# Optimization experiments

Measured on AMD Instinct MI355X. Metric: run time of the kernel, lower is better.

The kernel has to match this reference:

```python
import jax, jax.numpy as jnp
import numpy as np

N, NA, LAYERS = 8, 4, 4
NTOT = N + NA
DIM = 2 ** NTOT
B = 1024

# Diagonal of the fixed CZ brick layer (CZ is diagonal, so one elementwise pass per layer).
# Qubit 0 is the most-significant bit of the state index (tensorcircuit convention).
def _cz_diag():
    idx = np.arange(DIM)
    bits = (idx[None, :] >> (NTOT - 1 - np.arange(NTOT)[:, None])) & 1  # [NTOT, DIM]
    par = np.zeros(DIM, dtype=np.int64)
    for i in range(NTOT // 2):
        par += bits[2 * i] * bits[2 * i + 1]
    for i in range((NTOT - 1) // 2):
        par += bits[2 * i + 1] * bits[2 * i + 2]
    return jnp.asarray(1.0 - 2.0 * (par % 2), dtype=jnp.complex64)

CZ_DIAG = _cz_diag()

def _apply_1q(state, U, q):
    # state: [B, DIM]; apply 2x2 unitary U on qubit q (batched over samples)
    l, r = 2 ** q, 2 ** (NTOT - q - 1)
    s = state.reshape(-1, l, 2, r)
    return jnp.einsum('ij,bljr->blir', U, s).reshape(-1, DIM)

def _back_circuit(state, params):
    # hardware-efficient ansatz: per layer RX,RY on every qubit, then CZ bricks
    for lay in range(LAYERS):
        off = 2 * NTOT * lay
        for q in range(NTOT):
            th = params[off + q] * 0.5
            c = jnp.cos(th).astype(jnp.complex64)
            ms = (-1j) * jnp.sin(th).astype(jnp.complex64)
            Rx = jnp.stack([jnp.stack([c, ms]), jnp.stack([ms, c])])
            state = _apply_1q(state, Rx, q)
            th = params[off + NTOT + q] * 0.5
            c, s = jnp.cos(th), jnp.sin(th)
            Ry = jnp.stack([jnp.stack([c, -s]), jnp.stack([s, c])]).astype(jnp.complex64)
            state = _apply_1q(state, Ry, q)
        state = state * CZ_DIAG
    return state

def setup_inputs() -> dict:
    key = jax.random.key(0)
    k1, k2, k3, k4 = jax.random.split(key, 4)
    return {
        'inputs_re': jax.random.normal(k1, (B, DIM), jnp.float32),
        'inputs_im': jax.random.normal(k2, (B, DIM), jnp.float32),
        'params': jax.random.normal(k3, (2 * NTOT * LAYERS,), jnp.float32),
        'u': jax.random.uniform(k4, (B,), jnp.float32),
    }

def reference(inputs_re, inputs_im, params, u):
    state = (inputs_re + 1j * inputs_im).astype(jnp.complex64)
    full = _back_circuit(state, params)                      # [B, 2^n_tot]
    s3 = full.reshape(B, 2 ** NA, 2 ** N)                    # [B, 2^na, 2^n]
    probs = jnp.sum(s3.real ** 2 + s3.imag ** 2, axis=2)     # ancilla outcome probs
    cdf = jnp.cumsum(probs, axis=1)
    thresh = u * cdf[:, -1]                                  # inverse-CDF multinomial
    m = jnp.argmax(cdf >= thresh[:, None], axis=1)           # [B] sampled outcome
    post = s3[jnp.arange(B), m]                              # [B, 2^n] collapsed state
    norm = jnp.sqrt(jnp.sum(post.real ** 2 + post.imag ** 2, axis=1, keepdims=True))
    post = post / norm
    return jnp.stack([post.real, post.imag], axis=-1)        # [B, 2^n, 2]
```

## Files before the change

kernel.cpp:

```cpp
#include <hip/hip_runtime.h>
#include <math.h>

#define NTOT   12
#define DIM    4096
#define NB     1024

typedef float v2f __attribute__((ext_vector_type(2)));

template<int G>
__device__ __forceinline__ void gate_pk(v2f (&x)[16], v2f P1, v2f P2) {
#pragma unroll
    for (int p = 0; p < 8; ++p) {
        const int j0 = ((p >> G) << (G + 1)) | (p & ((1 << G) - 1));
        const int j1 = j0 | (1 << G);
        const v2f x0 = x[j0], x1 = x[j1];
        v2f t, u;
        asm("v_pk_mul_f32 %0, %1, %2 op_sel:[1,1] op_sel_hi:[1,0] neg_hi:[1,0]"
            : "=v"(t) : "v"(P2), "v"(x1));
        asm("v_pk_fma_f32 %0, %1, %2, %0 op_sel:[1,0,0] op_sel_hi:[1,1,1] neg_lo:[1,0,0] neg_hi:[1,0,0]"
            : "+v"(t) : "v"(P1), "v"(x1));
        asm("v_pk_fma_f32 %0, %1, %2, %0 op_sel:[0,1,0] op_sel_hi:[0,0,1] neg_lo:[1,0,0]"
            : "+v"(t) : "v"(P2), "v"(x0));
        asm("v_pk_fma_f32 %0, %1, %2, %0 op_sel:[0,0,0] op_sel_hi:[0,1,1]"
            : "+v"(t) : "v"(P1), "v"(x0));
        asm("v_pk_mul_f32 %0, %1, %2 op_sel:[0,1] op_sel_hi:[0,0] neg_hi:[1,0]"
            : "=v"(u) : "v"(P2), "v"(x1));
        asm("v_pk_fma_f32 %0, %1, %2, %0 op_sel:[0,0,0] op_sel_hi:[0,1,1]"
            : "+v"(u) : "v"(P1), "v"(x1));
        asm("v_pk_fma_f32 %0, %1, %2, %0 op_sel:[1,1,0] op_sel_hi:[1,0,1] neg_hi:[1,0,0]"
            : "+v"(u) : "v"(P2), "v"(x0));
        asm("v_pk_fma_f32 %0, %1, %2, %0 op_sel:[1,0,0] op_sel_hi:[1,1,1]"
            : "+v"(u) : "v"(P1), "v"(x0));
        x[j0] = t; x[j1] = u;
    }
}

__device__ __forceinline__ float rl(float v, int l) {
    return __int_as_float(__builtin_amdgcn_readlane(__float_as_int(v), l));
}

__device__ __forceinline__ void apply4(v2f (&x)[16],
                                       float gv0, float gv1, float gv2, float gv3,
                                       int base) {
    v2f P1, P2;
#define LDCO(GL) \
    P1.x = rl(gv0, (GL)); P1.y = rl(gv1, (GL)); \
    P2.x = rl(gv2, (GL)); P2.y = rl(gv3, (GL));
    LDCO(base + 3); gate_pk<0>(x, P1, P2);
    LDCO(base + 2); gate_pk<1>(x, P1, P2);
    LDCO(base + 1); gate_pk<2>(x, P1, P2);
    LDCO(base + 0); gate_pk<3>(x, P1, P2);
#undef LDCO
}

__device__ __forceinline__ void applyCZ(v2f (&x)[16], const int (&sw)[16]) {
#pragma unroll
    for (int j = 0; j < 16; ++j) {
        x[j].x = __uint_as_float(__float_as_uint(x[j].x) ^ sw[j]);
        x[j].y = __uint_as_float(__float_as_uint(x[j].y) ^ sw[j]);
    }
}

__global__ __launch_bounds__(256, 5) void qddpm_kernel(
    const float* __restrict__ in_re,
    const float* __restrict__ in_im,
    const float* __restrict__ params,
    const float* __restrict__ uu,
    float* __restrict__ out)
{
    __shared__ v2f S[DIM];

    const int b    = blockIdx.x;
    const int t    = threadIdx.x;
    const int lane = t & 63;
    const float uval = uu[b];

    const int hsC   = (t >> 1) & 7;
    const int baseC = t * 16;
    const int tA    = t ^ ((t >> 4) & 14);
    const int baseB = (t >> 4) * 256 + (t & 15);

    v2f x[16];

    {
        const float4* re4 = (const float4*)(in_re + (size_t)b * DIM + t * 16);
        const float4* im4 = (const float4*)(in_im + (size_t)b * DIM + t * 16);
#pragma unroll
        for (int q = 0; q < 4; ++q) {
            const float4 vr = re4[q];
            const float4 vi = im4[q];
            x[4 * q + 0] = (v2f){vr.x, vi.x};
            x[4 * q + 1] = (v2f){vr.y, vi.y};
            x[4 * q + 2] = (v2f){vr.z, vi.z};
            x[4 * q + 3] = (v2f){vr.w, vi.w};
        }
    }

    float gv0 = 0.f, gv1 = 0.f, gv2 = 0.f, gv3 = 0.f;
    if (lane < 48) {
        const int lay = lane / 12, q = lane - lay * 12;
        float c1, s1, c2, s2;
        sincosf(params[lay * 24 + q] * 0.5f, &s1, &c1);
        sincosf(params[lay * 24 + 12 + q] * 0.5f, &s2, &c2);
        gv0 = c1 * c2; gv1 = c1 * s2; gv2 = s1 * s2; gv3 = s1 * c2;
    }

    int swA[16], swC[16];
#pragma unroll
    for (int j = 0; j < 16; ++j) {
        const int iC = t * 16 + j;
        swC[j] = (__popc(iC & (iC >> 1) & 0x7FF) & 1) << 31;
        const int iA = j * 256 + t;
        swA[j] = (__popc(iA & (iA >> 1) & 0x7FF) & 1) << 31;
    }

#define C_WRITE() { float4* dst = (float4*)(S + baseC); \
    _Pragma("unroll") for (int q = 0; q < 8; ++q) \
        dst[q ^ hsC] = make_float4(x[2*q].x, x[2*q].y, x[2*q+1].x, x[2*q+1].y); }
#define C_READ() { const float4* src = (const float4*)(S + baseC); \
    _Pragma("unroll") for (int q = 0; q < 8; ++q) { const float4 v = src[q ^ hsC]; \
        x[2*q] = (v2f){v.x, v.y}; x[2*q+1] = (v2f){v.z, v.w}; } }
#define B_IDX(j) (baseB + (j) * 16 + (((t & 15) ^ ((j) & 14)) - (t & 15)))
#define B_READ()  { _Pragma("unroll") for (int j = 0; j < 16; ++j) x[j] = S[B_IDX(j)]; }
#define B_WRITE() { _Pragma("unroll") for (int j = 0; j < 16; ++j) S[B_IDX(j)] = x[j]; }
#define A_READ()  { _Pragma("unroll") for (int j = 0; j < 16; ++j) x[j] = S[j * 256 + tA]; }
#define A_WRITE() { _Pragma("unroll") for (int j = 0; j < 16; ++j) S[j * 256 + tA] = x[j]; }

    apply4(x, gv0, gv1, gv2, gv3, 0 * 12 + 8);
    C_WRITE();
    __syncthreads();

    B_READ();
    apply4(x, gv0, gv1, gv2, gv3, 0 * 12 + 4);
    B_WRITE();
    __syncthreads();

    A_READ();
    apply4(x, gv0, gv1, gv2, gv3, 0 * 12 + 0);
    applyCZ(x, swA);
    apply4(x, gv0, gv1, gv2, gv3, 1 * 12 + 0);
    A_WRITE();
    __syncthreads();

    B_READ();
    apply4(x, gv0, gv1, gv2, gv3, 1 * 12 + 4);
    B_WRITE();
    __syncthreads();

    C_READ();
    apply4(x, gv0, gv1, gv2, gv3, 1 * 12 + 8);
    applyCZ(x, swC);
    apply4(x, gv0, gv1, gv2, gv3, 2 * 12 + 8);
    C_WRITE();
    __syncthreads();

    B_READ();
    apply4(x, gv0, gv1, gv2, gv3, 2 * 12 + 4);
    B_WRITE();
    __syncthreads();

    A_READ();
    apply4(x, gv0, gv1, gv2, gv3, 2 * 12 + 0);
    applyCZ(x, swA);
    apply4(x, gv0, gv1, gv2, gv3, 3 * 12 + 0);
    A_WRITE();
    __syncthreads();

    B_READ();
    apply4(x, gv0, gv1, gv2, gv3, 3 * 12 + 4);
    B_WRITE();
    __syncthreads();

    C_READ();
    apply4(x, gv0, gv1, gv2, gv3, 3 * 12 + 8);
    applyCZ(x, swC);
    C_WRITE();
    __syncthreads();

    float partial = 0.f;
#pragma unroll
    for (int q = 0; q < 32; ++q) {
        const int qq = q ^ (lane & 31);
        const int X  = (lane * 4 + (qq >> 3)) & 14;
        const float4 v = ((const float4*)S)[lane * 32 + (qq ^ (X >> 1))];
        partial = __builtin_fmaf(v.x, v.x,
                  __builtin_fmaf(v.y, v.y,
                  __builtin_fmaf(v.z, v.z,
                  __builtin_fmaf(v.w, v.w, partial))));
    }
    partial += __shfl_xor(partial, 1);
    partial += __shfl_xor(partial, 2);

    float pr[16];
#pragma unroll
    for (int g = 0; g < 16; ++g) pr[g] = __shfl(partial, g * 4);

    float cdf[16];
    float a = 0.f;
#pragma unroll
    for (int g = 0; g < 16; ++g) { a += pr[g]; cdf[g] = a; }
    const float thresh = uval * a;
    int m = 0;
#pragma unroll
    for (int g = 15; g >= 0; --g) { if (cdf[g] >= thresh) m = g; }
    float pm = pr[0];
#pragma unroll
    for (int g = 1; g < 16; ++g) { if (m == g) pm = pr[g]; }
    const float rn = 1.0f / sqrtf(pm);

    const v2f amp = S[m * 256 + tA];
    ((float2*)out)[(size_t)b * 256 + t] = make_float2(amp.x * rn, amp.y * rn);
}

extern "C" void kernel_launch(void* const* d_in, const int* in_sizes, int n_in,
                              void* d_out, int out_size, void* d_ws, size_t ws_size,
                              hipStream_t stream) {
    const float* in_re  = (const float*)d_in[0];
    const float* in_im  = (const float*)d_in[1];
    const float* params = (const float*)d_in[2];
    const float* u      = (const float*)d_in[3];
    float* out = (float*)d_out;
    qddpm_kernel<<<NB, 256, 0, stream>>>(in_re, in_im, params, u, out);
}
```

Before: 115.3 us.

## Process two batch samples per block and finish from registers

```diff
diff --git a/kernel.cpp b/kernel.cpp
--- a/kernel.cpp
+++ b/kernel.cpp
@@ -4,6 +4,7 @@
 #define NTOT   12
 #define DIM    4096
 #define NB     1024
+#define NBLK   (NB / 2)
 
 typedef float v2f __attribute__((ext_vector_type(2)));
 
@@ -61,38 +62,86 @@
     }
 }
 
-__global__ __launch_bounds__(256, 5) void qddpm_kernel(
+__device__ __forceinline__ void c_write(v2f* S, const v2f (&x)[16], int t) {
+    float4* dst = (float4*)(S + t * 16);
+    const int hsC = (t >> 1) & 7;
+#pragma unroll
+    for (int q = 0; q < 8; ++q)
+        dst[q ^ hsC] = make_float4(x[2*q].x, x[2*q].y, x[2*q+1].x, x[2*q+1].y);
+}
+__device__ __forceinline__ void c_read(const v2f* S, v2f (&x)[16], int t) {
+    const float4* src = (const float4*)(S + t * 16);
+    const int hsC = (t >> 1) & 7;
+#pragma unroll
+    for (int q = 0; q < 8; ++q) {
+        const float4 v = src[q ^ hsC];
+        x[2*q]   = (v2f){v.x, v.y};
+        x[2*q+1] = (v2f){v.z, v.w};
+    }
+}
+__device__ __forceinline__ void b_read(const v2f* S, v2f (&x)[16], int t) {
+#pragma unroll
+    for (int j = 0; j < 16; ++j)
+        x[j] = S[(t >> 4) * 256 + j * 16 + ((t & 15) ^ (j & 14))];
+}
+__device__ __forceinline__ void b_write(v2f* S, const v2f (&x)[16], int t) {
+#pragma unroll
+    for (int j = 0; j < 16; ++j)
+        S[(t >> 4) * 256 + j * 16 + ((t & 15) ^ (j & 14))] = x[j];
+}
+__device__ __forceinline__ void a_read(const v2f* S, v2f (&x)[16], int tA) {
+#pragma unroll
+    for (int j = 0; j < 16; ++j) x[j] = S[j * 256 + tA];
+}
+__device__ __forceinline__ void a_write(v2f* S, const v2f (&x)[16], int tA) {
+#pragma unroll
+    for (int j = 0; j < 16; ++j) S[j * 256 + tA] = x[j];
+}
+
+__global__ __launch_bounds__(256, 2) void qddpm_kernel(
     const float* __restrict__ in_re,
     const float* __restrict__ in_im,
     const float* __restrict__ params,
     const float* __restrict__ uu,
     float* __restrict__ out)
 {
-    __shared__ v2f S[DIM];
-
-    const int b    = blockIdx.x;
+    __shared__ v2f SA[DIM];
+    __shared__ v2f SB[DIM];
+
+    const int blk  = blockIdx.x;
     const int t    = threadIdx.x;
     const int lane = t & 63;
-    const float uval = uu[b];
-
-    const int hsC   = (t >> 1) & 7;
-    const int baseC = t * 16;
-    const int tA    = t ^ ((t >> 4) & 14);
-    const int baseB = (t >> 4) * 256 + (t & 15);
-
-    v2f x[16];
+    const int bA   = 2 * blk;
+    const int bB   = 2 * blk + 1;
+    const int tA   = t ^ ((t >> 4) & 14);
+
+    const float uvalA = uu[bA];
+    const float uvalB = uu[bB];
+
+    v2f xA[16], xB[16];
 
     {
-        const float4* re4 = (const float4*)(in_re + (size_t)b * DIM + t * 16);
-        const float4* im4 = (const float4*)(in_im + (size_t)b * DIM + t * 16);
+        const float4* reA = (const float4*)(in_re + (size_t)bA * DIM + t * 16);
+        const float4* imA = (const float4*)(in_im + (size_t)bA * DIM + t * 16);
+        const float4* reB = (const float4*)(in_re + (size_t)bB * DIM + t * 16);
+        const float4* imB = (const float4*)(in_im + (size_t)bB * DIM + t * 16);
 #pragma unroll
         for (int q = 0; q < 4; ++q) {
-            const float4 vr = re4[q];
-            const float4 vi = im4[q];
-            x[4 * q + 0] = (v2f){vr.x, vi.x};
-            x[4 * q + 1] = (v2f){vr.y, vi.y};
-            x[4 * q + 2] = (v2f){vr.z, vi.z};
-            x[4 * q + 3] = (v2f){vr.w, vi.w};
+            const float4 vr = reA[q];
+            const float4 vi = imA[q];
+            xA[4*q+0] = (v2f){vr.x, vi.x};
+            xA[4*q+1] = (v2f){vr.y, vi.y};
+            xA[4*q+2] = (v2f){vr.z, vi.z};
+            xA[4*q+3] = (v2f){vr.w, vi.w};
+        }
+#pragma unroll
+        for (int q = 0; q < 4; ++q) {
+            const float4 vr = reB[q];
+            const float4 vi = imB[q];
+            xB[4*q+0] = (v2f){vr.x, vi.x};
+            xB[4*q+1] = (v2f){vr.y, vi.y};
+            xB[4*q+2] = (v2f){vr.z, vi.z};
+            xB[4*q+3] = (v2f){vr.w, vi.w};
         }
     }
 
@@ -114,102 +163,144 @@
         swA[j] = (__popc(iA & (iA >> 1) & 0x7FF) & 1) << 31;
     }
 
-#define C_WRITE() { float4* dst = (float4*)(S + baseC); \
-    _Pragma("unroll") for (int q = 0; q < 8; ++q) \
-        dst[q ^ hsC] = make_float4(x[2*q].x, x[2*q].y, x[2*q+1].x, x[2*q+1].y); }
-#define C_READ() { const float4* src = (const float4*)(S + baseC); \
-    _Pragma("unroll") for (int q = 0; q < 8; ++q) { const float4 v = src[q ^ hsC]; \
-        x[2*q] = (v2f){v.x, v.y}; x[2*q+1] = (v2f){v.z, v.w}; } }
-#define B_IDX(j) (baseB + (j) * 16 + (((t & 15) ^ ((j) & 14)) - (t & 15)))
-#define B_READ()  { _Pragma("unroll") for (int j = 0; j < 16; ++j) x[j] = S[B_IDX(j)]; }
-#define B_WRITE() { _Pragma("unroll") for (int j = 0; j < 16; ++j) S[B_IDX(j)] = x[j]; }
-#define A_READ()  { _Pragma("unroll") for (int j = 0; j < 16; ++j) x[j] = S[j * 256 + tA]; }
-#define A_WRITE() { _Pragma("unroll") for (int j = 0; j < 16; ++j) S[j * 256 + tA] = x[j]; }
-
-    apply4(x, gv0, gv1, gv2, gv3, 0 * 12 + 8);
-    C_WRITE();
-    __syncthreads();
-
-    B_READ();
-    apply4(x, gv0, gv1, gv2, gv3, 0 * 12 + 4);
-    B_WRITE();
-    __syncthreads();
-
-    A_READ();
-    apply4(x, gv0, gv1, gv2, gv3, 0 * 12 + 0);
-    applyCZ(x, swA);
-    apply4(x, gv0, gv1, gv2, gv3, 1 * 12 + 0);
-    A_WRITE();
-    __syncthreads();
-
-    B_READ();
-    apply4(x, gv0, gv1, gv2, gv3, 1 * 12 + 4);
-    B_WRITE();
-    __syncthreads();
-
-    C_READ();
-    apply4(x, gv0, gv1, gv2, gv3, 1 * 12 + 8);
-    applyCZ(x, swC);
-    apply4(x, gv0, gv1, gv2, gv3, 2 * 12 + 8);
-    C_WRITE();
-    __syncthreads();
-
-    B_READ();
-    apply4(x, gv0, gv1, gv2, gv3, 2 * 12 + 4);
-    B_WRITE();
-    __syncthreads();
-
-    A_READ();
-    apply4(x, gv0, gv1, gv2, gv3, 2 * 12 + 0);
-    applyCZ(x, swA);
-    apply4(x, gv0, gv1, gv2, gv3, 3 * 12 + 0);
-    A_WRITE();
-    __syncthreads();
-
-    B_READ();
-    apply4(x, gv0, gv1, gv2, gv3, 3 * 12 + 4);
-    B_WRITE();
-    __syncthreads();
-
-    C_READ();
-    apply4(x, gv0, gv1, gv2, gv3, 3 * 12 + 8);
-    applyCZ(x, swC);
-    C_WRITE();
-    __syncthreads();
-
-    float partial = 0.f;
-#pragma unroll
-    for (int q = 0; q < 32; ++q) {
-        const int qq = q ^ (lane & 31);
-        const int X  = (lane * 4 + (qq >> 3)) & 14;
-        const float4 v = ((const float4*)S)[lane * 32 + (qq ^ (X >> 1))];
-        partial = __builtin_fmaf(v.x, v.x,
-                  __builtin_fmaf(v.y, v.y,
-                  __builtin_fmaf(v.z, v.z,
-                  __builtin_fmaf(v.w, v.w, partial))));
-    }
-    partial += __shfl_xor(partial, 1);
-    partial += __shfl_xor(partial, 2);
-
-    float pr[16];
-#pragma unroll
-    for (int g = 0; g < 16; ++g) pr[g] = __shfl(partial, g * 4);
-
-    float cdf[16];
-    float a = 0.f;
-#pragma unroll
-    for (int g = 0; g < 16; ++g) { a += pr[g]; cdf[g] = a; }
-    const float thresh = uval * a;
-    int m = 0;
-#pragma unroll
-    for (int g = 15; g >= 0; --g) { if (cdf[g] >= thresh) m = g; }
-    float pm = pr[0];
-#pragma unroll
-    for (int g = 1; g < 16; ++g) { if (m == g) pm = pr[g]; }
-    const float rn = 1.0f / sqrtf(pm);
-
-    const v2f amp = S[m * 256 + tA];
-    ((float2*)out)[(size_t)b * 256 + t] = make_float2(amp.x * rn, amp.y * rn);
+    apply4(xA, gv0, gv1, gv2, gv3, 0 * 12 + 8);
+    c_write(SA, xA, t);
+    apply4(xB, gv0, gv1, gv2, gv3, 0 * 12 + 8);
+    c_write(SB, xB, t);
+    __syncthreads();
+
+    b_read(SA, xA, t);
+    b_read(SB, xB, t);
+    apply4(xA, gv0, gv1, gv2, gv3, 0 * 12 + 4);
+    b_write(SA, xA, t);
+    apply4(xB, gv0, gv1, gv2, gv3, 0 * 12 + 4);
+    b_write(SB, xB, t);
+    __syncthreads();
+
+    a_read(SA, xA, tA);
+    a_read(SB, xB, tA);
+    apply4(xA, gv0, gv1, gv2, gv3, 0 * 12 + 0);
+    applyCZ(xA, swA);
+    apply4(xA, gv0, gv1, gv2, gv3, 1 * 12 + 0);
+    a_write(SA, xA, tA);
+    apply4(xB, gv0, gv1, gv2, gv3, 0 * 12 + 0);
+    applyCZ(xB, swA);
+    apply4(xB, gv0, gv1, gv2, gv3, 1 * 12 + 0);
+    a_write(SB, xB, tA);
+    __syncthreads();
+
+    b_read(SA, xA, t);
+    b_read(SB, xB, t);
+    apply4(xA, gv0, gv1, gv2, gv3, 1 * 12 + 4);
+    b_write(SA, xA, t);
+    apply4(xB, gv0, gv1, gv2, gv3, 1 * 12 + 4);
+    b_write(SB, xB, t);
+    __syncthreads();
+
+    c_read(SA, xA, t);
+    c_read(SB, xB, t);
+    apply4(xA, gv0, gv1, gv2, gv3, 1 * 12 + 8);
+    applyCZ(xA, swC);
+    apply4(xA, gv0, gv1, gv2, gv3, 2 * 12 + 8);
+    c_write(SA, xA, t);
+    apply4(xB, gv0, gv1, gv2, gv3, 1 * 12 + 8);
+    applyCZ(xB, swC);
+    apply4(xB, gv0, gv1, gv2, gv3, 2 * 12 + 8);
+    c_write(SB, xB, t);
+    __syncthreads();
+
+    b_read(SA, xA, t);
+    b_read(SB, xB, t);
+    apply4(xA, gv0, gv1, gv2, gv3, 2 * 12 + 4);
+    b_write(SA, xA, t);
+    apply4(xB, gv0, gv1, gv2, gv3, 2 * 12 + 4);
+    b_write(SB, xB, t);
+    __syncthreads();
+
+    a_read(SA, xA, tA);
+    a_read(SB, xB, tA);
+    apply4(xA, gv0, gv1, gv2, gv3, 2 * 12 + 0);
+    applyCZ(xA, swA);
+    apply4(xA, gv0, gv1, gv2, gv3, 3 * 12 + 0);
+    a_write(SA, xA, tA);
+    apply4(xB, gv0, gv1, gv2, gv3, 2 * 12 + 0);
+    applyCZ(xB, swA);
+    apply4(xB, gv0, gv1, gv2, gv3, 3 * 12 + 0);
+    a_write(SB, xB, tA);
+    __syncthreads();
+
+    b_read(SA, xA, t);
+    b_read(SB, xB, t);
+    apply4(xA, gv0, gv1, gv2, gv3, 3 * 12 + 4);
+    b_write(SA, xA, t);
+    apply4(xB, gv0, gv1, gv2, gv3, 3 * 12 + 4);
+    b_write(SB, xB, t);
+    __syncthreads();
+
+    c_read(SA, xA, t);
+    c_read(SB, xB, t);
+    __syncthreads();
+
+    apply4(xA, gv0, gv1, gv2, gv3, 3 * 12 + 8);
+    applyCZ(xA, swC);
+    apply4(xB, gv0, gv1, gv2, gv3, 3 * 12 + 8);
+    applyCZ(xB, swC);
+
+    float pA, pB;
+    {
+        v2f accA = (v2f){0.f, 0.f}, accB = (v2f){0.f, 0.f};
+#pragma unroll
+        for (int j = 0; j < 16; ++j) { accA += xA[j] * xA[j]; accB += xB[j] * xB[j]; }
+        pA = accA.x + accA.y;
+        pB = accB.x + accB.y;
+#pragma unroll
+        for (int o = 8; o > 0; o >>= 1) {
+            pA += __shfl_down(pA, o, 16);
+            pB += __shfl_down(pB, o, 16);
+        }
+    }
+    if ((t & 15) == 0) {
+        ((float*)SA)[t >> 4] = pA;
+        ((float*)SB)[t >> 4] = pB;
+    }
+    __syncthreads();
+
+    {
+        const float* prA = (const float*)SA;
+        const float* prB = (const float*)SB;
+        float cdfA[16], cdfB[16];
+        float aA = 0.f, aB = 0.f;
+#pragma unroll
+        for (int i = 0; i < 16; ++i) {
+            aA += prA[i]; cdfA[i] = aA;
+            aB += prB[i]; cdfB[i] = aB;
+        }
+        const float thA = uvalA * aA;
+        const float thB = uvalB * aB;
+        int mA = 0, mB = 0;
+#pragma unroll
+        for (int i = 15; i >= 0; --i) {
+            if (cdfA[i] >= thA) mA = i;
+            if (cdfB[i] >= thB) mB = i;
+        }
+        const float rnA = 1.0f / sqrtf(prA[mA]);
+        const float rnB = 1.0f / sqrtf(prB[mB]);
+
+        if ((t >> 4) == mA) {
+            float4* o = (float4*)out + (size_t)bA * 128 + (t & 15) * 8;
+#pragma unroll
+            for (int q = 0; q < 8; ++q)
+                o[q] = make_float4(xA[2*q].x * rnA, xA[2*q].y * rnA,
+                                   xA[2*q+1].x * rnA, xA[2*q+1].y * rnA);
+        }
+        if ((t >> 4) == mB) {
+            float4* o = (float4*)out + (size_t)bB * 128 + (t & 15) * 8;
+#pragma unroll
+            for (int q = 0; q < 8; ++q)
+                o[q] = make_float4(xB[2*q].x * rnB, xB[2*q].y * rnB,
+                                   xB[2*q+1].x * rnB, xB[2*q+1].y * rnB);
+        }
+    }
 }
 
 extern "C" void kernel_launch(void* const* d_in, const int* in_sizes, int n_in,
@@ -220,5 +311,5 @@
     const float* params = (const float*)d_in[2];
     const float* u      = (const float*)d_in[3];
     float* out = (float*)d_out;
-    qddpm_kernel<<<NB, 256, 0, stream>>>(in_re, in_im, params, u, out);
-}
+    qddpm_kernel<<<NBLK, 256, 0, stream>>>(in_re, in_im, params, u, out);
+}
```

After: 113.1 us. Within noise of the previous version (-1.8%).
